# Kernel optimization log

Measured on AMD Instinct MI355X. Metric: run time of the kernel, lower is better.

Reference implementation:

```python
import jax, jax.numpy as jnp
import numpy as np

C = 6      # in_channel (forced by the module's own shape constraints)
MID = 3    # in_channel // 2
EPS = 1e-5


def setup_inputs() -> dict:
    key = jax.random.key(0)
    ks = jax.random.split(key, 16)
    B, N, NC, L = 2, 32768, 3, 2048
    w = lambda k, shape: jax.random.normal(k, shape, jnp.float32) * 0.2
    return {
        "x": jax.random.normal(ks[0], (B, C, N), jnp.float32),
        "curves": jax.random.normal(ks[1], (B, C, NC, L), jnp.float32),
        "Wa": w(ks[2], (MID, C)),    # conva   (Conv1d C->MID, k=1, no bias)
        "Wav": w(ks[3], (MID, C)),   # conva_v
        "Wb": w(ks[4], (MID, C)),    # convb
        "Wbv": w(ks[5], (MID, C)),   # convb_v
        "Wc": w(ks[6], (MID, C)),    # convc
        "Wd": w(ks[7], (C, 2 * MID)),  # convd Conv1d 2*MID -> C
        "bn_gamma": jnp.ones((C,), jnp.float32),
        "bn_beta": jnp.zeros((C,), jnp.float32),
        "Watt": w(ks[8], (C,)),      # line_conv_att Conv2d C->1, k=1
        "ln_gamma": jnp.ones((2 * MID,), jnp.float32),
        "ln_beta": jnp.zeros((2 * MID,), jnp.float32),
        "Wpl": w(ks[9], (MID, 3)),   # p_l Conv1d 3->MID (with bias)
        "bpl": w(ks[10], (MID,)),
        "Wpn": w(ks[11], (MID, 3)),  # p_n Conv1d 3->MID (with bias)
        "bpn": w(ks[12], (MID,)),
    }


def reference(x, curves, Wa, Wav, Wb, Wbv, Wc, Wd, bn_gamma, bn_beta,
              Watt, ln_gamma, ln_beta, Wpl, bpl, Wpn, bpn):
    # p, curve = curves  (tensor unpack along dim 0)
    p = curves[0]                                        # [C, 3, L]
    # p_l / p_n: Conv1d(3, MID) with p treated as batch=C, channels=3
    pl = jnp.einsum('bkl,mk->bml', p, Wpl) + bpl[None, :, None]   # [C, MID, L]
    p_l = pl.mean(axis=-1)                               # [C, MID]
    pn = jnp.einsum('bkl,mk->bml', p, Wpn) + bpn[None, :, None]   # [C, MID, L]
    p_n = pn.mean(axis=-2)                               # [C, L]

    # line attention over curves
    att = jnp.einsum('bcnl,c->bnl', curves, Watt)[:, None, :, :]  # [B,1,3,L]
    curver_inter = (curves * jax.nn.softmax(att, axis=-1)).sum(axis=-1)  # [B,C,3]
    curves_intra = (curves * jax.nn.softmax(att, axis=-2)).sum(axis=-2)  # [B,C,L]

    gi = curver_inter + p_l                              # [B,C,3] + [C,3(MID)]
    ga = curves_intra + p_n                              # [B,C,L] + [C,L]
    k_inter = jnp.einsum('bcn,mc->bmn', gi, Wa)          # [B,MID,3]
    v_inter = jnp.einsum('bcn,mc->bnm', gi, Wav)         # [B,3,MID]
    k_intra = jnp.einsum('bcl,mc->bml', ga, Wb)          # [B,MID,L]
    v_intra = jnp.einsum('bcl,mc->blm', ga, Wbv)         # [B,L,MID]

    q = jnp.einsum('bcn,mc->bnm', x, Wc)                 # [B,N,MID]
    scale = jnp.sqrt(jnp.float32(q.shape[-1]))           # sqrt(MID)

    att_inter = jax.nn.softmax(jnp.einsum('bnm,bmk->bnk', q, k_inter) / scale, axis=-1)
    feature_inter = jnp.einsum('bnk,bkm->bnm', att_inter, v_inter)   # [B,N,MID]
    att_intra = jax.nn.softmax(jnp.einsum('bnm,bml->bnl', q, k_intra) / scale, axis=-1)
    feature_intra = jnp.einsum('bnl,blm->bnm', att_intra, v_intra)   # [B,N,MID]

    cf = jnp.concatenate([feature_inter, feature_intra], axis=-1)    # [B,N,2*MID]
    mu = cf.mean(axis=-1, keepdims=True)
    var = ((cf - mu) ** 2).mean(axis=-1, keepdims=True)
    cf = (cf - mu) * jax.lax.rsqrt(var + EPS) * ln_gamma + ln_beta   # LayerNorm
    cf = jnp.swapaxes(cf, 1, 2)                                      # [B,2*MID,N]

    y = jnp.einsum('bcn,oc->bon', cf, Wd)                # Conv1d 2*MID -> C
    # BatchNorm1d (training-mode batch statistics over (B, N))
    bm = y.mean(axis=(0, 2), keepdims=True)
    bv = ((y - bm) ** 2).mean(axis=(0, 2), keepdims=True)
    y = (y - bm) * jax.lax.rsqrt(bv + EPS) * bn_gamma[None, :, None] + bn_beta[None, :, None]

    out = x + y
    return jnp.where(out >= 0, out, 0.2 * out)           # LeakyReLU(0.2)
```

## Files before the change

### kernel.cpp

```cpp
#include <hip/hip_runtime.h>
#include <math.h>

#define N_PTS 32768
#define LL    2048

#define KT_U      0
#define VT_U      8192
#define PART_OFF  16384
#define MS_OFF    28672
#define W_OFF     28684
#define CS_OFF    28720
#define PBKM_OFF  28738
#define BNS_OFF   28762
#define BNB_OFF   28768

typedef __fp16 h2    __attribute__((ext_vector_type(2)));
typedef __fp16 f16x4 __attribute__((ext_vector_type(4)));
typedef float  f32x4 __attribute__((ext_vector_type(4)));

__device__ __forceinline__ unsigned h2_bits(h2 h){
  union { h2 h; unsigned u; } x; x.h = h; return x.u;
}
__device__ __forceinline__ float wave_reduce_sum(float v){
  #pragma unroll
  for (int off = 32; off; off >>= 1) v += __shfl_xor(v, off, 64);
  return v;
}
__device__ __forceinline__ float wave_reduce_max(float v){
  #pragma unroll
  for (int off = 32; off; off >>= 1) v = fmaxf(v, __shfl_xor(v, off, 64));
  return v;
}

__global__ __launch_bounds__(256)
void prep_kernel(const float* __restrict__ curves, const float* __restrict__ Watt,
                 const float* __restrict__ Wb,  const float* __restrict__ Wbv,
                 const float* __restrict__ Wpn, const float* __restrict__ bpn,
                 float* __restrict__ ws)
{
  const int blk = blockIdx.x, tid = threadIdx.x;
  const int lane = tid & 63, wid = tid >> 6;
  __shared__ float sred[4 * 13];
  __shared__ float msh;

  float watt[6];
  #pragma unroll
  for (int c = 0; c < 6; c++) watt[c] = Watt[c];

  if (blk < 6) {
    const int b = blk / 3, nc = blk % 3;
    const float* cb = curves + b * 18 * LL;
    float av[8], pm = -1e30f;
    #pragma unroll
    for (int k = 0; k < 8; k++) {
      const int l = tid + k * 256;
      float s = 0.f;
      #pragma unroll
      for (int c = 0; c < 6; c++) s = fmaf(cb[(c * 3 + nc) * LL + l], watt[c], s);
      av[k] = s; pm = fmaxf(pm, s);
    }
    pm = wave_reduce_max(pm);
    if (lane == 0) sred[wid] = pm;
    __syncthreads();
    if (tid == 0) msh = fmaxf(fmaxf(sred[0], sred[1]), fmaxf(sred[2], sred[3]));
    __syncthreads();
    const float m = msh;

    float vals[13];
    #pragma unroll
    for (int j = 0; j < 13; j++) vals[j] = 0.f;
    #pragma unroll
    for (int k = 0; k < 8; k++) {
      const int l = tid + k * 256;
      float e = __expf(av[k] - m);
      vals[0] += e;
      #pragma unroll
      for (int c = 0; c < 6; c++) {
        float v = cb[(c * 3 + nc) * LL + l];
        vals[1 + c] = fmaf(v, e, vals[1 + c]);
        if (b == 0) vals[7 + c] += v;
      }
    }
    __syncthreads();
    #pragma unroll
    for (int j = 0; j < 13; j++) vals[j] = wave_reduce_sum(vals[j]);
    if (lane == 0) { for (int j = 0; j < 13; j++) sred[wid * 13 + j] = vals[j]; }
    __syncthreads();
    if (tid == 0) {
      ws[MS_OFF + blk * 2] = m;
      for (int j = 0; j < 13; j++) {
        float s = sred[j] + sred[13 + j] + sred[26 + j] + sred[39 + j];
        if (j == 0) ws[MS_OFF + blk * 2 + 1] = s;
        else if (j < 7) ws[W_OFF + blk * 6 + (j - 1)] = s;
        else if (b == 0) ws[CS_OFF + nc * 6 + (j - 7)] = s;
      }
    }
  } else {
    const int idx = (blk - 6) * 256 + tid;
    const int b = idx >> 10, pp = idx & 1023, l = pp * 2;
    const float* cb = curves + b * 18 * LL;

    float2 cv[6][3], pv[6][3];
    #pragma unroll
    for (int c = 0; c < 6; c++)
      #pragma unroll
      for (int nc = 0; nc < 3; nc++) {
        cv[c][nc] = *(const float2*)&cb[(c * 3 + nc) * LL + l];
        pv[c][nc] = *(const float2*)&curves[(c * 3 + nc) * LL + l];
      }
    float a[3][2];
    #pragma unroll
    for (int nc = 0; nc < 3; nc++) {
      float sx = 0.f, sy = 0.f;
      #pragma unroll
      for (int c = 0; c < 6; c++) {
        sx = fmaf(cv[c][nc].x, watt[c], sx);
        sy = fmaf(cv[c][nc].y, watt[c], sy);
      }
      a[nc][0] = sx; a[nc][1] = sy;
    }

    float wb_r[18], wbv_r[18];
    #pragma unroll
    for (int i = 0; i < 18; i++) { wb_r[i] = Wb[i]; wbv_r[i] = Wbv[i]; }
    const float wn0 = (Wpn[0] + Wpn[3] + Wpn[6]) * (1.f / 3.f);
    const float wn1 = (Wpn[1] + Wpn[4] + Wpn[7]) * (1.f / 3.f);
    const float wn2 = (Wpn[2] + Wpn[5] + Wpn[8]) * (1.f / 3.f);
    const float bnb = (bpn[0] + bpn[1] + bpn[2]) * (1.f / 3.f);

    float kk[2][3], vv[2][3], km[3] = {0.f, 0.f, 0.f};
    #pragma unroll
    for (int e = 0; e < 2; e++) {
      float a0 = a[0][e], a1 = a[1][e], a2 = a[2][e];
      float mm = fmaxf(fmaxf(a0, a1), a2);
      float e0 = __expf(a0 - mm), e1 = __expf(a1 - mm), e2 = __expf(a2 - mm);
      float r = 1.f / (e0 + e1 + e2);
      float ga[6];
      #pragma unroll
      for (int c = 0; c < 6; c++) {
        float c0 = e ? cv[c][0].y : cv[c][0].x;
        float c1 = e ? cv[c][1].y : cv[c][1].x;
        float c2 = e ? cv[c][2].y : cv[c][2].x;
        float p0 = e ? pv[c][0].y : pv[c][0].x;
        float p1 = e ? pv[c][1].y : pv[c][1].x;
        float p2 = e ? pv[c][2].y : pv[c][2].x;
        float intra = (c0 * e0 + c1 * e1 + c2 * e2) * r;
        float pn = p0 * wn0 + p1 * wn1 + p2 * wn2 + bnb;
        ga[c] = intra + pn;
      }
      float k0 = 0, k1 = 0, k2 = 0, v0 = 0, v1 = 0, v2 = 0;
      #pragma unroll
      for (int c = 0; c < 6; c++) {
        k0 += wb_r[c] * ga[c];  k1 += wb_r[6 + c] * ga[c];  k2 += wb_r[12 + c] * ga[c];
        v0 += wbv_r[c] * ga[c]; v1 += wbv_r[6 + c] * ga[c]; v2 += wbv_r[12 + c] * ga[c];
      }
      kk[e][0] = k0; kk[e][1] = k1; kk[e][2] = k2;
      vv[e][0] = v0; vv[e][1] = v1; vv[e][2] = v2;
      km[0] = fmaxf(km[0], fabsf(k0));
      km[1] = fmaxf(km[1], fabsf(k1));
      km[2] = fmaxf(km[2], fabsf(k2));
    }
    unsigned* ktg = (unsigned*)ws + KT_U + b * 4096;
    ktg[4 * pp + 0] = h2_bits(__builtin_amdgcn_cvt_pkrtz(kk[0][0], kk[0][1]));
    ktg[4 * pp + 1] = h2_bits(__builtin_amdgcn_cvt_pkrtz(kk[0][2], 0.f));
    ktg[4 * pp + 2] = h2_bits(__builtin_amdgcn_cvt_pkrtz(kk[1][0], kk[1][1]));
    ktg[4 * pp + 3] = h2_bits(__builtin_amdgcn_cvt_pkrtz(kk[1][2], 0.f));
    unsigned* vtg = (unsigned*)ws + VT_U + b * 4096;
    vtg[0 * 1024 + pp] = h2_bits(__builtin_amdgcn_cvt_pkrtz(vv[0][0], vv[1][0]));
    vtg[1 * 1024 + pp] = h2_bits(__builtin_amdgcn_cvt_pkrtz(vv[0][1], vv[1][1]));
    vtg[2 * 1024 + pp] = h2_bits(__builtin_amdgcn_cvt_pkrtz(vv[0][2], vv[1][2]));
    vtg[3 * 1024 + pp] = h2_bits(__builtin_amdgcn_cvt_pkrtz(1.f, 1.f));

    #pragma unroll
    for (int j = 0; j < 3; j++) km[j] = wave_reduce_max(km[j]);
    if (lane == 0) { for (int j = 0; j < 3; j++) sred[wid * 3 + j] = km[j]; }
    __syncthreads();
    if (tid == 0) {
      for (int j = 0; j < 3; j++)
        ws[PBKM_OFF + (blk - 6) * 3 + j] =
          fmaxf(fmaxf(sred[j], sred[3 + j]), fmaxf(sred[6 + j], sred[9 + j]));
    }
  }
}

__global__ __launch_bounds__(256, 4)
void attn_kernel(const float* __restrict__ x,  const float* __restrict__ Wc,
                 const float* __restrict__ Wd, const float* __restrict__ lng,
                 const float* __restrict__ lnb,
                 const float* __restrict__ Wa, const float* __restrict__ Wav,
                 const float* __restrict__ Wpl, const float* __restrict__ bpl,
                 float* __restrict__ ws, float* __restrict__ yout)
{
  __shared__ __align__(16) unsigned kt[4224];
  __shared__ __align__(16) unsigned vt[4224];
  __shared__ float4 cross[2][64];
  __shared__ float gis[18], kis[9], vis[9];
  const int tid  = threadIdx.x, blk = blockIdx.x;
  const int lane = tid & 63, w = tid >> 6;
  const int col  = lane & 15, hi4 = lane >> 4;
  const int rp   = w >> 1, kh = w & 1;
  const int rbase = blk * 64;
  const int b    = rbase >> 15;
  const int nb   = rbase & (N_PTS - 1);

  {
    const uint4* ktg = (const uint4*)((const unsigned*)ws + KT_U + b * 4096);
    uint4* kt4 = (uint4*)kt;
    for (int i = tid; i < 1024; i += 256) kt4[i] = ktg[i];
    const uint2* vtg2 = (const uint2*)((const unsigned*)ws + VT_U + b * 4096);
    for (int i = tid; i < 2048; i += 256) {
      int pl = i >> 9, off = (i & 511) << 1;
      *(uint2*)&vt[pl * 1028 + off] = vtg2[i];
    }
    if (tid < 2) { kt[4096 + tid] = 0; vt[4112 + tid] = 0; }
  }
  if (tid < 18) {
    int c = tid / 3, m = tid % 3;
    float pl_ = bpl[m];
    #pragma unroll
    for (int k = 0; k < 3; k++)
      pl_ = fmaf(Wpl[m * 3 + k], ws[CS_OFF + k * 6 + c] * (1.f / LL), pl_);
    gis[c * 3 + m] = ws[W_OFF + (b * 3 + m) * 6 + c] / ws[MS_OFF + (b * 3 + m) * 2 + 1] + pl_;
  }
  __syncthreads();
  if (tid < 9) {
    int m = tid / 3, k = tid % 3;
    float s1 = 0.f, s2 = 0.f;
    #pragma unroll
    for (int c = 0; c < 6; c++) {
      float g = gis[c * 3 + k];
      s1 = fmaf(Wa [m * 6 + c], g, s1);
      s2 = fmaf(Wav[m * 6 + c], g, s2);
    }
    kis[m * 3 + k] = s1; vis[k * 3 + m] = s2;
  }

  float km0 = 0.f, km1 = 0.f, km2 = 0.f;
  #pragma unroll
  for (int s = 0; s < 4; s++) {
    const float* pk = ws + PBKM_OFF + (b * 4 + s) * 3;
    km0 = fmaxf(km0, pk[0]); km1 = fmaxf(km1, pk[1]); km2 = fmaxf(km2, pk[2]);
  }

  const int nA = nb + rp * 32 + col, nBr = nA + 16;
  const float* xb = x + (size_t)b * 6 * N_PTS;
  float q0A = 0, q1A = 0, q2A = 0, q0B = 0, q1B = 0, q2B = 0;
  #pragma unroll
  for (int c = 0; c < 6; c++) {
    float xvA = xb[c * N_PTS + nA], xvB = xb[c * N_PTS + nBr];
    q0A = fmaf(xvA, Wc[c], q0A); q1A = fmaf(xvA, Wc[6 + c], q1A); q2A = fmaf(xvA, Wc[12 + c], q2A);
    q0B = fmaf(xvB, Wc[c], q0B); q1B = fmaf(xvB, Wc[6 + c], q1B); q2B = fmaf(xvB, Wc[12 + c], q2B);
  }
  const float KS = 1.4426950408889634f * 0.57735026918962576f;
  q0A *= KS; q1A *= KS; q2A *= KS; q0B *= KS; q1B *= KS; q2B *= KS;
  const float MpA = fabsf(q0A) * km0 + fabsf(q1A) * km1 + fabsf(q2A) * km2;
  const float MpB = fabsf(q0B) * km0 + fabsf(q1B) * km1 + fabsf(q2B) * km2;

  union U2 { uint2 u; f16x4 h; };
  U2 qbA, qbB;
  qbA.u.x = qbA.u.y = qbB.u.x = qbB.u.y = 0;
  if (hi4 == 0) {
    qbA.u.x = h2_bits(__builtin_amdgcn_cvt_pkrtz(q0A, q1A));
    qbA.u.y = h2_bits(__builtin_amdgcn_cvt_pkrtz(q2A, 0.f));
    qbB.u.x = h2_bits(__builtin_amdgcn_cvt_pkrtz(q0B, q1B));
    qbB.u.y = h2_bits(__builtin_amdgcn_cvt_pkrtz(q2B, 0.f));
  }
  f32x4 cbA = { -MpA, -MpA, -MpA, -MpA };
  f32x4 cbB = { -MpB, -MpB, -MpB, -MpB };
  f32x4 aA0 = {0,0,0,0}, aA1 = {0,0,0,0}, aB0 = {0,0,0,0}, aB1 = {0,0,0,0};

  unsigned ki_ = (hi4 == 0) ? (unsigned)(kh * 2048 + col * 2) : 4096u;
  const unsigned kd = (hi4 == 0) ? 32u : 0u;
  unsigned vi_ = (col < 4) ? (unsigned)(col * 1028 + kh * 512 + 2 * hi4) : 4112u;
  const unsigned vd = (col < 4) ? 8u : 0u;

  U2 Kc, Vc;
  Kc.u = *(const uint2*)&kt[ki_];
  Vc.u = *(const uint2*)&vt[vi_];

  #pragma unroll 4
  for (int i = 0; i < 64; i++) {
    ki_ += kd; vi_ += vd;
    U2 Kn, Vn;
    Kn.u = *(const uint2*)&kt[ki_];
    Vn.u = *(const uint2*)&vt[vi_];
    f32x4 sA = __builtin_amdgcn_mfma_f32_16x16x16f16(Kc.h, qbA.h, cbA, 0, 0, 0);
    f32x4 sB = __builtin_amdgcn_mfma_f32_16x16x16f16(Kc.h, qbB.h, cbB, 0, 0, 0);
    float eA0 = __builtin_amdgcn_exp2f(sA[0]);
    float eA1 = __builtin_amdgcn_exp2f(sA[1]);
    float eA2 = __builtin_amdgcn_exp2f(sA[2]);
    float eA3 = __builtin_amdgcn_exp2f(sA[3]);
    float eB0 = __builtin_amdgcn_exp2f(sB[0]);
    float eB1 = __builtin_amdgcn_exp2f(sB[1]);
    float eB2 = __builtin_amdgcn_exp2f(sB[2]);
    float eB3 = __builtin_amdgcn_exp2f(sB[3]);
    U2 PA, PB;
    PA.u.x = h2_bits(__builtin_amdgcn_cvt_pkrtz(eA0, eA1));
    PA.u.y = h2_bits(__builtin_amdgcn_cvt_pkrtz(eA2, eA3));
    PB.u.x = h2_bits(__builtin_amdgcn_cvt_pkrtz(eB0, eB1));
    PB.u.y = h2_bits(__builtin_amdgcn_cvt_pkrtz(eB2, eB3));
    if (i & 1) {
      aA1 = __builtin_amdgcn_mfma_f32_16x16x16f16(Vc.h, PA.h, aA1, 0, 0, 0);
      aB1 = __builtin_amdgcn_mfma_f32_16x16x16f16(Vc.h, PB.h, aB1, 0, 0, 0);
    } else {
      aA0 = __builtin_amdgcn_mfma_f32_16x16x16f16(Vc.h, PA.h, aA0, 0, 0, 0);
      aB0 = __builtin_amdgcn_mfma_f32_16x16x16f16(Vc.h, PB.h, aB0, 0, 0, 0);
    }
    Kc = Kn; Vc = Vn;
  }

  if (hi4 == 0) {
    cross[kh][rp * 32 + col] =
      make_float4(aA0[0] + aA1[0], aA0[1] + aA1[1], aA0[2] + aA1[2], aA0[3] + aA1[3]);
    cross[kh][rp * 32 + 16 + col] =
      make_float4(aB0[0] + aB1[0], aB0[1] + aB1[1], aB0[2] + aB1[2], aB0[3] + aB1[3]);
  }
  __syncthreads();

  if (tid < 64) {
    const int ri = tid, n = nb + ri;
    float4 c0 = cross[0][ri], c1 = cross[1][ri];
    float w0 = c0.x + c1.x, w1 = c0.y + c1.y, w2 = c0.z + c1.z, dd = c0.w + c1.w;

    float a0 = 0, a1 = 0, a2 = 0;
    #pragma unroll
    for (int c = 0; c < 6; c++) {
      float xv = xb[c * N_PTS + n];
      a0 = fmaf(xv, Wc[c], a0); a1 = fmaf(xv, Wc[6 + c], a1); a2 = fmaf(xv, Wc[12 + c], a2);
    }
    a0 *= KS; a1 *= KS; a2 *= KS;

    float sk0 = a0 * kis[0] + a1 * kis[3] + a2 * kis[6];
    float sk1 = a0 * kis[1] + a1 * kis[4] + a2 * kis[7];
    float sk2 = a0 * kis[2] + a1 * kis[5] + a2 * kis[8];
    float mm  = fmaxf(fmaxf(sk0, sk1), sk2);
    float e0 = __builtin_amdgcn_exp2f(sk0 - mm);
    float e1 = __builtin_amdgcn_exp2f(sk1 - mm);
    float e2 = __builtin_amdgcn_exp2f(sk2 - mm);
    float rs = 1.f / (e0 + e1 + e2);
    float fi0 = (e0 * vis[0] + e1 * vis[3] + e2 * vis[6]) * rs;
    float fi1 = (e0 * vis[1] + e1 * vis[4] + e2 * vis[7]) * rs;
    float fi2 = (e0 * vis[2] + e1 * vis[5] + e2 * vis[8]) * rs;
    float rinv = 1.f / dd;
    float cf[6] = { fi0, fi1, fi2, w0 * rinv, w1 * rinv, w2 * rinv };

    float mu = (cf[0] + cf[1] + cf[2] + cf[3] + cf[4] + cf[5]) * (1.f / 6.f);
    float var = 0.f;
    #pragma unroll
    for (int i = 0; i < 6; i++) { float t = cf[i] - mu; var += t * t; }
    var *= (1.f / 6.f);
    float rn = rsqrtf(var + 1e-5f);
    float cfn[6];
    #pragma unroll
    for (int i = 0; i < 6; i++) cfn[i] = (cf[i] - mu) * rn * lng[i] + lnb[i];

    float v12[12];
    #pragma unroll
    for (int o = 0; o < 6; o++) {
      float s = 0.f;
      #pragma unroll
      for (int c = 0; c < 6; c++) s += Wd[o * 6 + c] * cfn[c];
      yout[(size_t)b * (6 * N_PTS) + o * N_PTS + n] = s;
      v12[o] = s; v12[6 + o] = s * s;
    }
    #pragma unroll
    for (int j = 0; j < 12; j++) v12[j] = wave_reduce_sum(v12[j]);
    if (tid == 0) {
      float* part = ws + PART_OFF + blk * 12;
      for (int j = 0; j < 12; j++) part[j] = v12[j];
    }
  }
}

__global__ __launch_bounds__(256)
void bnstats_kernel(const float* __restrict__ bng, const float* __restrict__ bnbt,
                    float* __restrict__ ws)
{
  __shared__ float cp[48];
  const int tid = threadIdx.x;
  const float* part = ws + PART_OFF;
  float v[12];
  #pragma unroll
  for (int j = 0; j < 12; j++)
    v[j] = part[tid * 12 + j] + part[(tid + 256) * 12 + j]
         + part[(tid + 512) * 12 + j] + part[(tid + 768) * 12 + j];
  #pragma unroll
  for (int j = 0; j < 12; j++) v[j] = wave_reduce_sum(v[j]);
  const int lane = tid & 63, wid = tid >> 6;
  if (lane == 0) { for (int j = 0; j < 12; j++) cp[wid * 12 + j] = v[j]; }
  __syncthreads();
  if (tid == 0) {
    const float inv = 1.f / 65536.f;
    for (int o = 0; o < 6; o++) {
      float s1 = cp[o] + cp[12 + o] + cp[24 + o] + cp[36 + o];
      float s2 = cp[6 + o] + cp[18 + o] + cp[30 + o] + cp[42 + o];
      float mean = s1 * inv;
      float varr = s2 * inv - mean * mean;
      float sc = bng[o] * rsqrtf(varr + 1e-5f);
      ws[BNS_OFF + o] = sc;
      ws[BNB_OFF + o] = bnbt[o] - mean * sc;
    }
  }
}

__global__ __launch_bounds__(256)
void final_kernel(const float* __restrict__ x, const float* __restrict__ ws,
                  float* __restrict__ out)
{
  const int i = blockIdx.x * 256 + threadIdx.x;
  const int ch = (i >> 15) % 6;
  float v = out[i] * ws[BNS_OFF + ch] + ws[BNB_OFF + ch] + x[i];
  out[i] = v >= 0.f ? v : 0.2f * v;
}

extern "C" void kernel_launch(void* const* d_in, const int* in_sizes, int n_in,
                              void* d_out, int out_size, void* d_ws, size_t ws_size,
                              hipStream_t stream)
{
  const float* x      = (const float*)d_in[0];
  const float* curves = (const float*)d_in[1];
  const float* Wa     = (const float*)d_in[2];
  const float* Wav    = (const float*)d_in[3];
  const float* Wb     = (const float*)d_in[4];
  const float* Wbv    = (const float*)d_in[5];
  const float* Wc     = (const float*)d_in[6];
  const float* Wd     = (const float*)d_in[7];
  const float* bng    = (const float*)d_in[8];
  const float* bnbt   = (const float*)d_in[9];
  const float* Watt   = (const float*)d_in[10];
  const float* lng    = (const float*)d_in[11];
  const float* lnbt   = (const float*)d_in[12];
  const float* Wpl    = (const float*)d_in[13];
  const float* bpl    = (const float*)d_in[14];
  const float* Wpn    = (const float*)d_in[15];
  const float* bpn    = (const float*)d_in[16];
  float* out = (float*)d_out;
  float* ws  = (float*)d_ws;

  prep_kernel<<<14, 256, 0, stream>>>(curves, Watt, Wb, Wbv, Wpn, bpn, ws);
  attn_kernel<<<1024, 256, 0, stream>>>(x, Wc, Wd, lng, lnbt,
                                        Wa, Wav, Wpl, bpl, ws, out);
  bnstats_kernel<<<1, 256, 0, stream>>>(bng, bnbt, ws);
  final_kernel<<<1536, 256, 0, stream>>>(x, ws, out);
}
```

Baseline: 34.55 us.

## Split attention key dimension four ways per wave, each wave handling all row tiles

Each of the four waves now covers one quarter of the 2048 keys for all 64 query rows (four 16-row tiles), where before two row pairs split the keys in halves. Each K/V fragment loaded from LDS is therefore reused across four MFMAs instead of two, and the loop trip count halves. s_setprio is raised around the MFMA groups to favour matrix issue over the exp work of other waves. The cost is more accumulator and query registers per thread and a four-way cross-wave reduction through shared memory.

Measured after the change: 36.35 us. 5.2% more time.

```diff
diff --git a/kernel.cpp b/kernel.cpp
--- a/kernel.cpp
+++ b/kernel.cpp
@@ -193,12 +193,11 @@
 {
   __shared__ __align__(16) unsigned kt[4224];
   __shared__ __align__(16) unsigned vt[4224];
-  __shared__ float4 cross[2][64];
+  __shared__ float4 cross[4][64];
   __shared__ float gis[18], kis[9], vis[9];
   const int tid  = threadIdx.x, blk = blockIdx.x;
-  const int lane = tid & 63, w = tid >> 6;
+  const int lane = tid & 63, kq = tid >> 6;
   const int col  = lane & 15, hi4 = lane >> 4;
-  const int rp   = w >> 1, kh = w & 1;
   const int rbase = blk * 64;
   const int b    = rbase >> 15;
   const int nb   = rbase & (N_PTS - 1);
@@ -242,85 +241,98 @@
     km0 = fmaxf(km0, pk[0]); km1 = fmaxf(km1, pk[1]); km2 = fmaxf(km2, pk[2]);
   }
 
-  const int nA = nb + rp * 32 + col, nBr = nA + 16;
+  const float KS = 1.4426950408889634f * 0.57735026918962576f;
   const float* xb = x + (size_t)b * 6 * N_PTS;
-  float q0A = 0, q1A = 0, q2A = 0, q0B = 0, q1B = 0, q2B = 0;
-  #pragma unroll
-  for (int c = 0; c < 6; c++) {
-    float xvA = xb[c * N_PTS + nA], xvB = xb[c * N_PTS + nBr];
-    q0A = fmaf(xvA, Wc[c], q0A); q1A = fmaf(xvA, Wc[6 + c], q1A); q2A = fmaf(xvA, Wc[12 + c], q2A);
-    q0B = fmaf(xvB, Wc[c], q0B); q1B = fmaf(xvB, Wc[6 + c], q1B); q2B = fmaf(xvB, Wc[12 + c], q2B);
-  }
-  const float KS = 1.4426950408889634f * 0.57735026918962576f;
-  q0A *= KS; q1A *= KS; q2A *= KS; q0B *= KS; q1B *= KS; q2B *= KS;
-  const float MpA = fabsf(q0A) * km0 + fabsf(q1A) * km1 + fabsf(q2A) * km2;
-  const float MpB = fabsf(q0B) * km0 + fabsf(q1B) * km1 + fabsf(q2B) * km2;
 
   union U2 { uint2 u; f16x4 h; };
-  U2 qbA, qbB;
-  qbA.u.x = qbA.u.y = qbB.u.x = qbB.u.y = 0;
-  if (hi4 == 0) {
-    qbA.u.x = h2_bits(__builtin_amdgcn_cvt_pkrtz(q0A, q1A));
-    qbA.u.y = h2_bits(__builtin_amdgcn_cvt_pkrtz(q2A, 0.f));
-    qbB.u.x = h2_bits(__builtin_amdgcn_cvt_pkrtz(q0B, q1B));
-    qbB.u.y = h2_bits(__builtin_amdgcn_cvt_pkrtz(q2B, 0.f));
-  }
-  f32x4 cbA = { -MpA, -MpA, -MpA, -MpA };
-  f32x4 cbB = { -MpB, -MpB, -MpB, -MpB };
-  f32x4 aA0 = {0,0,0,0}, aA1 = {0,0,0,0}, aB0 = {0,0,0,0}, aB1 = {0,0,0,0};
-
-  unsigned ki_ = (hi4 == 0) ? (unsigned)(kh * 2048 + col * 2) : 4096u;
+  U2 qb[4];
+  f32x4 cb[4];
+  f32x4 acc0[4], acc1[4];
+  #pragma unroll
+  for (int rt = 0; rt < 4; rt++) {
+    const int n = nb + rt * 16 + col;
+    float q0 = 0, q1 = 0, q2 = 0;
+    #pragma unroll
+    for (int c = 0; c < 6; c++) {
+      float xv = xb[c * N_PTS + n];
+      q0 = fmaf(xv, Wc[c], q0); q1 = fmaf(xv, Wc[6 + c], q1); q2 = fmaf(xv, Wc[12 + c], q2);
+    }
+    q0 *= KS; q1 *= KS; q2 *= KS;
+    float Mp = fabsf(q0) * km0 + fabsf(q1) * km1 + fabsf(q2) * km2;
+    qb[rt].u.x = qb[rt].u.y = 0;
+    if (hi4 == 0) {
+      qb[rt].u.x = h2_bits(__builtin_amdgcn_cvt_pkrtz(q0, q1));
+      qb[rt].u.y = h2_bits(__builtin_amdgcn_cvt_pkrtz(q2, 0.f));
+    }
+    cb[rt] = (f32x4){ -Mp, -Mp, -Mp, -Mp };
+    acc0[rt] = (f32x4){0,0,0,0};
+    acc1[rt] = (f32x4){0,0,0,0};
+  }
+
+  unsigned ki_ = (hi4 == 0) ? (unsigned)(kq * 1024 + col * 2) : 4096u;
   const unsigned kd = (hi4 == 0) ? 32u : 0u;
-  unsigned vi_ = (col < 4) ? (unsigned)(col * 1028 + kh * 512 + 2 * hi4) : 4112u;
+  unsigned vi_ = (col < 4) ? (unsigned)(col * 1028 + kq * 256 + 2 * hi4) : 4112u;
   const unsigned vd = (col < 4) ? 8u : 0u;
 
   U2 Kc, Vc;
   Kc.u = *(const uint2*)&kt[ki_];
   Vc.u = *(const uint2*)&vt[vi_];
 
-  #pragma unroll 4
-  for (int i = 0; i < 64; i++) {
+  #pragma unroll 2
+  for (int i = 0; i < 32; i++) {
     ki_ += kd; vi_ += vd;
     U2 Kn, Vn;
     Kn.u = *(const uint2*)&kt[ki_];
     Vn.u = *(const uint2*)&vt[vi_];
-    f32x4 sA = __builtin_amdgcn_mfma_f32_16x16x16f16(Kc.h, qbA.h, cbA, 0, 0, 0);
-    f32x4 sB = __builtin_amdgcn_mfma_f32_16x16x16f16(Kc.h, qbB.h, cbB, 0, 0, 0);
-    float eA0 = __builtin_amdgcn_exp2f(sA[0]);
-    float eA1 = __builtin_amdgcn_exp2f(sA[1]);
-    float eA2 = __builtin_amdgcn_exp2f(sA[2]);
-    float eA3 = __builtin_amdgcn_exp2f(sA[3]);
-    float eB0 = __builtin_amdgcn_exp2f(sB[0]);
-    float eB1 = __builtin_amdgcn_exp2f(sB[1]);
-    float eB2 = __builtin_amdgcn_exp2f(sB[2]);
-    float eB3 = __builtin_amdgcn_exp2f(sB[3]);
-    U2 PA, PB;
-    PA.u.x = h2_bits(__builtin_amdgcn_cvt_pkrtz(eA0, eA1));
-    PA.u.y = h2_bits(__builtin_amdgcn_cvt_pkrtz(eA2, eA3));
-    PB.u.x = h2_bits(__builtin_amdgcn_cvt_pkrtz(eB0, eB1));
-    PB.u.y = h2_bits(__builtin_amdgcn_cvt_pkrtz(eB2, eB3));
+
+    f32x4 s[4];
+    __builtin_amdgcn_s_setprio(1);
+    #pragma unroll
+    for (int rt = 0; rt < 4; rt++)
+      s[rt] = __builtin_amdgcn_mfma_f32_16x16x16f16(Kc.h, qb[rt].h, cb[rt], 0, 0, 0);
+    __builtin_amdgcn_s_setprio(0);
+
+    U2 P[4];
+    #pragma unroll
+    for (int rt = 0; rt < 4; rt++) {
+      float e0 = __builtin_amdgcn_exp2f(s[rt][0]);
+      float e1 = __builtin_amdgcn_exp2f(s[rt][1]);
+      float e2 = __builtin_amdgcn_exp2f(s[rt][2]);
+      float e3 = __builtin_amdgcn_exp2f(s[rt][3]);
+      P[rt].u.x = h2_bits(__builtin_amdgcn_cvt_pkrtz(e0, e1));
+      P[rt].u.y = h2_bits(__builtin_amdgcn_cvt_pkrtz(e2, e3));
+    }
+
+    __builtin_amdgcn_s_setprio(1);
     if (i & 1) {
-      aA1 = __builtin_amdgcn_mfma_f32_16x16x16f16(Vc.h, PA.h, aA1, 0, 0, 0);
-      aB1 = __builtin_amdgcn_mfma_f32_16x16x16f16(Vc.h, PB.h, aB1, 0, 0, 0);
+      #pragma unroll
+      for (int rt = 0; rt < 4; rt++)
+        acc1[rt] = __builtin_amdgcn_mfma_f32_16x16x16f16(Vc.h, P[rt].h, acc1[rt], 0, 0, 0);
     } else {
-      aA0 = __builtin_amdgcn_mfma_f32_16x16x16f16(Vc.h, PA.h, aA0, 0, 0, 0);
-      aB0 = __builtin_amdgcn_mfma_f32_16x16x16f16(Vc.h, PB.h, aB0, 0, 0, 0);
-    }
+      #pragma unroll
+      for (int rt = 0; rt < 4; rt++)
+        acc0[rt] = __builtin_amdgcn_mfma_f32_16x16x16f16(Vc.h, P[rt].h, acc0[rt], 0, 0, 0);
+    }
+    __builtin_amdgcn_s_setprio(0);
     Kc = Kn; Vc = Vn;
   }
 
   if (hi4 == 0) {
-    cross[kh][rp * 32 + col] =
-      make_float4(aA0[0] + aA1[0], aA0[1] + aA1[1], aA0[2] + aA1[2], aA0[3] + aA1[3]);
-    cross[kh][rp * 32 + 16 + col] =
-      make_float4(aB0[0] + aB1[0], aB0[1] + aB1[1], aB0[2] + aB1[2], aB0[3] + aB1[3]);
+    #pragma unroll
+    for (int rt = 0; rt < 4; rt++)
+      cross[kq][rt * 16 + col] = make_float4(
+        acc0[rt][0] + acc1[rt][0], acc0[rt][1] + acc1[rt][1],
+        acc0[rt][2] + acc1[rt][2], acc0[rt][3] + acc1[rt][3]);
   }
   __syncthreads();
 
   if (tid < 64) {
     const int ri = tid, n = nb + ri;
-    float4 c0 = cross[0][ri], c1 = cross[1][ri];
-    float w0 = c0.x + c1.x, w1 = c0.y + c1.y, w2 = c0.z + c1.z, dd = c0.w + c1.w;
+    float4 c0 = cross[0][ri], c1 = cross[1][ri], c2 = cross[2][ri], c3 = cross[3][ri];
+    float w0 = c0.x + c1.x + c2.x + c3.x;
+    float w1 = c0.y + c1.y + c2.y + c3.y;
+    float w2 = c0.z + c1.z + c2.z + c3.z;
+    float dd = c0.w + c1.w + c2.w + c3.w;
 
     float a0 = 0, a1 = 0, a2 = 0;
     #pragma unroll
```

## Software-pipeline attention MFMA loop and fuse BN stats into final kernel

Applied to the files above, without the earlier changes.

The attention inner loop is software-pipelined so the score MFMAs for the next key tile are issued before the exp2 and PV MFMAs of the current tile, with a peeled epilogue. This hides MFMA latency behind the exponentials. The separate single-block BN-statistics kernel is merged into the final elementwise kernel: each of 384 blocks redundantly reduces the 1024 partials and then applies BN, residual add and LeakyReLU with float4 accesses. This drops one launch and its serialization, at the cost of every block re-reading the partials.

Measured after the change: 34.38 us. Within noise of the previous version (-0.5%).

```diff
diff --git a/kernel.cpp b/kernel.cpp
--- a/kernel.cpp
+++ b/kernel.cpp
@@ -274,26 +274,29 @@
   unsigned vi_ = (col < 4) ? (unsigned)(col * 1028 + kh * 512 + 2 * hi4) : 4112u;
   const unsigned vd = (col < 4) ? 8u : 0u;
 
-  U2 Kc, Vc;
+  U2 Kc, Vc, Kn, Vn;
   Kc.u = *(const uint2*)&kt[ki_];
   Vc.u = *(const uint2*)&vt[vi_];
-
-  #pragma unroll 4
-  for (int i = 0; i < 64; i++) {
-    ki_ += kd; vi_ += vd;
-    U2 Kn, Vn;
+  ki_ += kd; vi_ += vd;
+  Kn.u = *(const uint2*)&kt[ki_];
+  Vn.u = *(const uint2*)&vt[vi_];
+  f32x4 sAc = __builtin_amdgcn_mfma_f32_16x16x16f16(Kc.h, qbA.h, cbA, 0, 0, 0);
+  f32x4 sBc = __builtin_amdgcn_mfma_f32_16x16x16f16(Kc.h, qbB.h, cbB, 0, 0, 0);
+
+  #pragma unroll 2
+  for (int i = 0; i < 62; i++) {
+    f32x4 sAn = __builtin_amdgcn_mfma_f32_16x16x16f16(Kn.h, qbA.h, cbA, 0, 0, 0);
+    f32x4 sBn = __builtin_amdgcn_mfma_f32_16x16x16f16(Kn.h, qbB.h, cbB, 0, 0, 0);
+    ki_ += kd;
     Kn.u = *(const uint2*)&kt[ki_];
-    Vn.u = *(const uint2*)&vt[vi_];
-    f32x4 sA = __builtin_amdgcn_mfma_f32_16x16x16f16(Kc.h, qbA.h, cbA, 0, 0, 0);
-    f32x4 sB = __builtin_amdgcn_mfma_f32_16x16x16f16(Kc.h, qbB.h, cbB, 0, 0, 0);
-    float eA0 = __builtin_amdgcn_exp2f(sA[0]);
-    float eA1 = __builtin_amdgcn_exp2f(sA[1]);
-    float eA2 = __builtin_amdgcn_exp2f(sA[2]);
-    float eA3 = __builtin_amdgcn_exp2f(sA[3]);
-    float eB0 = __builtin_amdgcn_exp2f(sB[0]);
-    float eB1 = __builtin_amdgcn_exp2f(sB[1]);
-    float eB2 = __builtin_amdgcn_exp2f(sB[2]);
-    float eB3 = __builtin_amdgcn_exp2f(sB[3]);
+    float eA0 = __builtin_amdgcn_exp2f(sAc[0]);
+    float eA1 = __builtin_amdgcn_exp2f(sAc[1]);
+    float eA2 = __builtin_amdgcn_exp2f(sAc[2]);
+    float eA3 = __builtin_amdgcn_exp2f(sAc[3]);
+    float eB0 = __builtin_amdgcn_exp2f(sBc[0]);
+    float eB1 = __builtin_amdgcn_exp2f(sBc[1]);
+    float eB2 = __builtin_amdgcn_exp2f(sBc[2]);
+    float eB3 = __builtin_amdgcn_exp2f(sBc[3]);
     U2 PA, PB;
     PA.u.x = h2_bits(__builtin_amdgcn_cvt_pkrtz(eA0, eA1));
     PA.u.y = h2_bits(__builtin_amdgcn_cvt_pkrtz(eA2, eA3));
@@ -306,7 +309,38 @@
       aA0 = __builtin_amdgcn_mfma_f32_16x16x16f16(Vc.h, PA.h, aA0, 0, 0, 0);
       aB0 = __builtin_amdgcn_mfma_f32_16x16x16f16(Vc.h, PB.h, aB0, 0, 0, 0);
     }
-    Kc = Kn; Vc = Vn;
+    Vc = Vn;
+    vi_ += vd;
+    Vn.u = *(const uint2*)&vt[vi_];
+    sAc = sAn; sBc = sBn;
+  }
+  {
+    f32x4 sAn = __builtin_amdgcn_mfma_f32_16x16x16f16(Kn.h, qbA.h, cbA, 0, 0, 0);
+    f32x4 sBn = __builtin_amdgcn_mfma_f32_16x16x16f16(Kn.h, qbB.h, cbB, 0, 0, 0);
+    #pragma unroll
+    for (int e = 0; e < 2; e++) {
+      float e0 = __builtin_amdgcn_exp2f(sAc[0]);
+      float e1 = __builtin_amdgcn_exp2f(sAc[1]);
+      float e2 = __builtin_amdgcn_exp2f(sAc[2]);
+      float e3 = __builtin_amdgcn_exp2f(sAc[3]);
+      float f0 = __builtin_amdgcn_exp2f(sBc[0]);
+      float f1 = __builtin_amdgcn_exp2f(sBc[1]);
+      float f2 = __builtin_amdgcn_exp2f(sBc[2]);
+      float f3 = __builtin_amdgcn_exp2f(sBc[3]);
+      U2 PA, PB;
+      PA.u.x = h2_bits(__builtin_amdgcn_cvt_pkrtz(e0, e1));
+      PA.u.y = h2_bits(__builtin_amdgcn_cvt_pkrtz(e2, e3));
+      PB.u.x = h2_bits(__builtin_amdgcn_cvt_pkrtz(f0, f1));
+      PB.u.y = h2_bits(__builtin_amdgcn_cvt_pkrtz(f2, f3));
+      if (e == 0) {
+        aA0 = __builtin_amdgcn_mfma_f32_16x16x16f16(Vc.h, PA.h, aA0, 0, 0, 0);
+        aB0 = __builtin_amdgcn_mfma_f32_16x16x16f16(Vc.h, PB.h, aB0, 0, 0, 0);
+        Vc = Vn; sAc = sAn; sBc = sBn;
+      } else {
+        aA1 = __builtin_amdgcn_mfma_f32_16x16x16f16(Vc.h, PA.h, aA1, 0, 0, 0);
+        aB1 = __builtin_amdgcn_mfma_f32_16x16x16f16(Vc.h, PB.h, aB1, 0, 0, 0);
+      }
+    }
   }
 
   if (hi4 == 0) {
@@ -373,44 +407,51 @@
 }
 
 __global__ __launch_bounds__(256)
-void bnstats_kernel(const float* __restrict__ bng, const float* __restrict__ bnbt,
-                    float* __restrict__ ws)
+void final_kernel(const float* __restrict__ x,
+                  const float* __restrict__ bng, const float* __restrict__ bnbt,
+                  const float* __restrict__ ws, float* __restrict__ out)
 {
   __shared__ float cp[48];
-  const int tid = threadIdx.x;
+  __shared__ float sc_s[6], sh_s[6];
+  const int tid = threadIdx.x, blk = blockIdx.x;
+  const int lane = tid & 63, wid = tid >> 6;
   const float* part = ws + PART_OFF;
+
   float v[12];
   #pragma unroll
-  for (int j = 0; j < 12; j++)
-    v[j] = part[tid * 12 + j] + part[(tid + 256) * 12 + j]
-         + part[(tid + 512) * 12 + j] + part[(tid + 768) * 12 + j];
+  for (int j = 0; j < 12; j++) v[j] = 0.f;
+  #pragma unroll
+  for (int k = 0; k < 4; k++) {
+    const float* p = part + (tid * 4 + k) * 12;
+    #pragma unroll
+    for (int j = 0; j < 12; j++) v[j] += p[j];
+  }
   #pragma unroll
   for (int j = 0; j < 12; j++) v[j] = wave_reduce_sum(v[j]);
-  const int lane = tid & 63, wid = tid >> 6;
   if (lane == 0) { for (int j = 0; j < 12; j++) cp[wid * 12 + j] = v[j]; }
   __syncthreads();
-  if (tid == 0) {
+  if (tid < 6) {
     const float inv = 1.f / 65536.f;
-    for (int o = 0; o < 6; o++) {
-      float s1 = cp[o] + cp[12 + o] + cp[24 + o] + cp[36 + o];
-      float s2 = cp[6 + o] + cp[18 + o] + cp[30 + o] + cp[42 + o];
-      float mean = s1 * inv;
-      float varr = s2 * inv - mean * mean;
-      float sc = bng[o] * rsqrtf(varr + 1e-5f);
-      ws[BNS_OFF + o] = sc;
-      ws[BNB_OFF + o] = bnbt[o] - mean * sc;
-    }
-  }
-}
-
-__global__ __launch_bounds__(256)
-void final_kernel(const float* __restrict__ x, const float* __restrict__ ws,
-                  float* __restrict__ out)
-{
-  const int i = blockIdx.x * 256 + threadIdx.x;
-  const int ch = (i >> 15) % 6;
-  float v = out[i] * ws[BNS_OFF + ch] + ws[BNB_OFF + ch] + x[i];
-  out[i] = v >= 0.f ? v : 0.2f * v;
+    float s1 = cp[tid] + cp[12 + tid] + cp[24 + tid] + cp[36 + tid];
+    float s2 = cp[6 + tid] + cp[18 + tid] + cp[30 + tid] + cp[42 + tid];
+    float mean = s1 * inv;
+    float varr = s2 * inv - mean * mean;
+    float sc = bng[tid] * rsqrtf(varr + 1e-5f);
+    sc_s[tid] = sc;
+    sh_s[tid] = bnbt[tid] - mean * sc;
+  }
+  __syncthreads();
+
+  const int base = blk * 1024 + tid * 4;
+  const int ch = (base >> 15) % 6;
+  const float sc = sc_s[ch], sh = sh_s[ch];
+  float4 o = *(float4*)&out[base];
+  float4 xx = *(const float4*)&x[base];
+  float r[4] = { o.x * sc + sh + xx.x, o.y * sc + sh + xx.y,
+                 o.z * sc + sh + xx.z, o.w * sc + sh + xx.w };
+  #pragma unroll
+  for (int j = 0; j < 4; j++) r[j] = r[j] >= 0.f ? r[j] : 0.2f * r[j];
+  *(float4*)&out[base] = make_float4(r[0], r[1], r[2], r[3]);
 }
 
 extern "C" void kernel_launch(void* const* d_in, const int* in_sizes, int n_in,
@@ -440,6 +481,5 @@
   prep_kernel<<<14, 256, 0, stream>>>(curves, Watt, Wb, Wbv, Wpn, bpn, ws);
   attn_kernel<<<1024, 256, 0, stream>>>(x, Wc, Wd, lng, lnbt,
                                         Wa, Wav, Wpl, bpl, ws, out);
-  bnstats_kernel<<<1, 256, 0, stream>>>(bng, bnbt, ws);
-  final_kernel<<<1536, 256, 0, stream>>>(x, ws, out);
-}
+  final_kernel<<<384, 256, 0, stream>>>(x, bng, bnbt, ws, out);
+}
```
